# Kernel optimization log

Measured on AMD Instinct MI355X. Metric: run time of the kernel, lower is better.

Reference implementation:

```python
import jax, jax.numpy as jnp
import numpy as np

N_NODES = 100000
N_EDGES = 625000
D = 128
N_LAYERS = 10

def setup_inputs() -> dict:
    key = jax.random.key(0)
    ks = jax.random.split(key, 6)
    x = jax.random.normal(ks[0], (N_NODES, D), dtype=jnp.float32)
    edge_index = jax.random.randint(ks[1], (2, N_EDGES), 0, N_NODES, dtype=jnp.int32)
    # PyG SAGEConv params per layer: lin_l (aggregated msgs, with bias), lin_r (root, no bias)
    scale = 1.0 / np.sqrt(D)
    Wl = jax.random.normal(ks[2], (N_LAYERS, D, D), dtype=jnp.float32) * scale
    Wr = jax.random.normal(ks[3], (N_LAYERS, D, D), dtype=jnp.float32) * scale
    b = jax.random.normal(ks[4], (N_LAYERS, D), dtype=jnp.float32) * 0.01
    return {"x": x, "Wl": Wl, "Wr": Wr, "b": b, "edge_index": edge_index}

def reference(x, Wl, Wr, b, edge_index):
    src = edge_index[0]
    dst = edge_index[1]
    n = x.shape[0]
    # in-degree for mean aggregation (clamped to avoid div by zero)
    deg = jax.ops.segment_sum(jnp.ones(src.shape[0], x.dtype), dst, num_segments=n)
    deg = jnp.maximum(deg, 1.0)[:, None]
    n_layers = Wl.shape[0]
    for i in range(n_layers):
        # SAGEConv: out = lin_l(mean_{j in N(i)} x_j) + lin_r(x_i)
        agg = jax.ops.segment_sum(x[src], dst, num_segments=n) / deg
        x = agg @ Wl[i] + x @ Wr[i] + b[i]
        if i < n_layers - 1:
            x = jax.nn.relu(x)  # dropout is identity in eval mode
    return x
```

## Files before the change

kernel.cpp:

```cpp
#include <hip/hip_runtime.h>
#include <hip/hip_bf16.h>

#define N_NODES 100000
#define N_EDGES 625000
#define D 128
#define N_LAYERS 10
#define SCAN_BLOCKS 98

typedef __attribute__((ext_vector_type(8))) short bf16x8;
typedef __attribute__((ext_vector_type(4))) float floatx4;

static __device__ __forceinline__ ushort f2bf(float f) {
    uint u = __float_as_uint(f);
    u += 0x7fff + ((u >> 16) & 1);
    return (ushort)(u >> 16);
}
static __device__ __forceinline__ float bf2f(ushort h) {
    return __uint_as_float(((uint)h) << 16);
}


__global__ void hist_kernel(const int* __restrict__ dst, int* __restrict__ deg) {
    int e = blockIdx.x * blockDim.x + threadIdx.x;
    if (e < N_EDGES) atomicAdd(&deg[dst[e]], 1);
}

__global__ void scanA_kernel(const int* __restrict__ deg, int* __restrict__ offsets,
                             int* __restrict__ blockSums) {
    __shared__ int s[1024];
    int tid = threadIdx.x;
    int i = blockIdx.x * 1024 + tid;
    int v = (i < N_NODES) ? deg[i] : 0;
    s[tid] = v;
    __syncthreads();
    for (int d = 1; d < 1024; d <<= 1) {
        int t = (tid >= d) ? s[tid - d] : 0;
        __syncthreads();
        s[tid] += t;
        __syncthreads();
    }
    if (i < N_NODES) offsets[i] = s[tid] - v;
    if (tid == 1023) blockSums[blockIdx.x] = s[1023];
}

__global__ void scanB_kernel(const int* __restrict__ blockSums, int* __restrict__ blockOffsets) {
    __shared__ int s[128];
    int tid = threadIdx.x;
    int v = (tid < SCAN_BLOCKS) ? blockSums[tid] : 0;
    s[tid] = v;
    __syncthreads();
    for (int d = 1; d < 128; d <<= 1) {
        int t = (tid >= d) ? s[tid - d] : 0;
        __syncthreads();
        s[tid] += t;
        __syncthreads();
    }
    blockOffsets[tid] = s[tid] - v;
}

__global__ void scanC_kernel(int* __restrict__ offsets, const int* __restrict__ blockOffsets) {
    int i = blockIdx.x * 1024 + threadIdx.x;
    if (i < N_NODES) offsets[i] += blockOffsets[blockIdx.x];
}

__global__ void invdeg_kernel(const int* __restrict__ deg, float* __restrict__ invdeg,
                              int* __restrict__ offsets) {
    int i = blockIdx.x * blockDim.x + threadIdx.x;
    if (i < N_NODES) {
        int d = deg[i];
        invdeg[i] = 1.0f / (float)(d > 0 ? d : 1);
    }
    if (i == 0) offsets[N_NODES] = N_EDGES;
}

__global__ void scatter_kernel(const int* __restrict__ src, const int* __restrict__ dst,
                               const int* __restrict__ offsets, int* __restrict__ fill,
                               int* __restrict__ srcSorted) {
    int e = blockIdx.x * blockDim.x + threadIdx.x;
    if (e < N_EDGES) {
        int d_ = dst[e];
        int pos = offsets[d_] + atomicAdd(&fill[d_], 1);
        srcSorted[pos] = src[e];
    }
}

__global__ void wsplit_kernel(const float* __restrict__ Wl, const float* __restrict__ Wr,
                              ushort* __restrict__ Whi, ushort* __restrict__ Wlo) {
    int t = blockIdx.x * blockDim.x + threadIdx.x;
    if (t >= N_LAYERS * 4 * 16 * 64) return;
    int lane  = t & 63;
    int ntile = (t >> 6) & 15;
    int s     = (t >> 10) & 3;
    int layer = t >> 12;
    int n = ntile * 16 + (lane & 15);
    int kbase = s * 32 + (lane >> 4) * 8;
    const float* W = (n < 128) ? (Wl + (size_t)layer * D * D + n)
                               : (Wr + (size_t)layer * D * D + (n - 128));
    size_t off = (size_t)t * 8;
#pragma unroll
    for (int j = 0; j < 8; ++j) {
        float w = W[(size_t)(kbase + j) * D];
        ushort hh = f2bf(w);
        Whi[off + j] = hh;
        Wlo[off + j] = f2bf(w - bf2f(hh));
    }
}

__global__ __launch_bounds__(256) void gemm_hz(
        const float* __restrict__ X, const ushort* __restrict__ Whi,
        const ushort* __restrict__ Wlo, const float* __restrict__ bias,
        uint* __restrict__ h2out, float* __restrict__ z) {
    __shared__ ushort Ahi[2][4 * 64 * 8];
    __shared__ ushort Alo[2][4 * 64 * 8];

    int tid  = threadIdx.x;
    int lane = tid & 63;
    int wave = tid >> 6;

    int r    = tid >> 4;
    int t0   = tid & 15;
    int s_st = t0 >> 2;
    int q_st = t0 & 3;
    int lanep = (q_st << 4) | r;
    int stIdx = (s_st * 64 + (lanep ^ (s_st << 2))) * 8;

    int q  = lane >> 4;
    int cc = lane & 15;

    int ntileMap[4];
#pragma unroll
    for (int nt = 0; nt < 4; ++nt)
        ntileMap[nt] = (wave < 2) ? (wave * 2 + (nt & 1) + ((nt >> 1) << 2))
                                  : (wave * 4 + nt);

    float bsc[4] = {0.f, 0.f, 0.f, 0.f};
    if (wave >= 2) {
#pragma unroll
        for (int nt = 0; nt < 4; ++nt)
            bsc[nt] = bias[((wave * 4 + nt) - 8) * 16 + cc];
    }

    int mt = blockIdx.x;
    {
        int row0 = mt * 32;
#pragma unroll
        for (int st = 0; st < 2; ++st) {
            const float* xp = X + (size_t)(row0 + st * 16 + r) * D + t0 * 8;
            float4 v0 = *(const float4*)xp;
            float4 v1 = *(const float4*)(xp + 4);
            float a[8] = {v0.x, v0.y, v0.z, v0.w, v1.x, v1.y, v1.z, v1.w};
            ushort hi8[8], lo8[8];
#pragma unroll
            for (int j = 0; j < 8; ++j) {
                ushort hh = f2bf(a[j]);
                hi8[j] = hh;
                lo8[j] = f2bf(a[j] - bf2f(hh));
            }
            *(bf16x8*)&Ahi[st][stIdx] = *(bf16x8*)hi8;
            *(bf16x8*)&Alo[st][stIdx] = *(bf16x8*)lo8;
        }
        __syncthreads();

        floatx4 acc0[4], acc1[4];
#pragma unroll
        for (int nt = 0; nt < 4; ++nt) {
            acc0[nt] = (floatx4){0.f, 0.f, 0.f, 0.f};
            acc1[nt] = (floatx4){0.f, 0.f, 0.f, 0.f};
        }
#pragma unroll
        for (int s = 0; s < 4; ++s) {
            int aIdx = (s * 64 + (lane ^ (s << 2))) * 8;
            bf16x8 ah0 = *(const bf16x8*)&Ahi[0][aIdx];
            bf16x8 al0 = *(const bf16x8*)&Alo[0][aIdx];
            bf16x8 ah1 = *(const bf16x8*)&Ahi[1][aIdx];
            bf16x8 al1 = *(const bf16x8*)&Alo[1][aIdx];
#pragma unroll
            for (int nt = 0; nt < 4; ++nt) {
                size_t wo = ((size_t)(s * 16 + ntileMap[nt]) * 64 + lane) * 8;
                bf16x8 wh = *(const bf16x8*)&Whi[wo];
                bf16x8 wl = *(const bf16x8*)&Wlo[wo];
                acc0[nt] = __builtin_amdgcn_mfma_f32_16x16x32_bf16(ah0, wh, acc0[nt], 0, 0, 0);
                acc0[nt] = __builtin_amdgcn_mfma_f32_16x16x32_bf16(al0, wh, acc0[nt], 0, 0, 0);
                acc0[nt] = __builtin_amdgcn_mfma_f32_16x16x32_bf16(ah0, wl, acc0[nt], 0, 0, 0);
                acc1[nt] = __builtin_amdgcn_mfma_f32_16x16x32_bf16(ah1, wh, acc1[nt], 0, 0, 0);
                acc1[nt] = __builtin_amdgcn_mfma_f32_16x16x32_bf16(al1, wh, acc1[nt], 0, 0, 0);
                acc1[nt] = __builtin_amdgcn_mfma_f32_16x16x32_bf16(ah1, wl, acc1[nt], 0, 0, 0);
            }
        }

#pragma unroll
        for (int st = 0; st < 2; ++st) {
            floatx4* acc = st ? acc1 : acc0;
            int rowb = row0 + st * 16;
            if (wave < 2) {
#pragma unroll
                for (int p = 0; p < 2; ++p) {
                    int c = wave * 32 + p * 16 + cc;
#pragma unroll
                    for (int rr = 0; rr < 4; ++rr) {
                        uint lo = f2bf(acc[p][rr]);
                        uint hi = f2bf(acc[p + 2][rr]);
                        h2out[(size_t)(rowb + q * 4 + rr) * 64 + c] = lo | (hi << 16);
                    }
                }
            } else {
#pragma unroll
                for (int nt = 0; nt < 4; ++nt) {
                    int col = ((wave * 4 + nt) - 8) * 16 + cc;
#pragma unroll
                    for (int rr = 0; rr < 4; ++rr) {
                        int row = rowb + q * 4 + rr;
                        z[(size_t)row * D + col] = acc[nt][rr] + bsc[nt];
                    }
                }
            }
        }
    }
}

__global__ __launch_bounds__(256) void fused_layer(
        const uint* __restrict__ h2in, const int* __restrict__ srcSorted,
        const int* __restrict__ offsets, const float* __restrict__ invdeg,
        const float* __restrict__ zio, const ushort* __restrict__ Whi,
        const ushort* __restrict__ Wlo, const float* __restrict__ bias,
        uint* __restrict__ h2out) {
    __shared__ ushort Ahi[2][4 * 64 * 8];
    __shared__ ushort Alo[2][4 * 64 * 8];

    int tid  = threadIdx.x;
    int lane = tid & 63;
    int wave = tid >> 6;
    int row0 = blockIdx.x * 32;

    int n0 = row0 + wave * 8;
    int offA[9];
#pragma unroll
    for (int i = 0; i < 9; ++i) offA[i] = offsets[n0 + i];
    int off0 = offA[0];
    int total = offA[8] - off0;
    int idxv = srcSorted[min(off0 + ((lane < total) ? lane : 0), N_EDGES - 1)];

    for (int i = 0; i < 8; ++i) {
        int sRel = offA[i] - off0;
        int eRel = offA[i + 1] - off0;
        int cnt = eRel - sRel;
        float sx = 0.f, sy = 0.f;
        if (cnt > 0 && eRel <= 64) {
            for (int k = sRel; k < eRel; k += 8) {
                int sidx[8];
#pragma unroll
                for (int j = 0; j < 8; ++j) {
                    int kk = k + j;
                    sidx[j] = __shfl(idxv, (kk < eRel) ? kk : sRel, 64);
                }
                uint u[8];
#pragma unroll
                for (int j = 0; j < 8; ++j)
                    u[j] = h2in[(size_t)sidx[j] * 64 + lane];
#pragma unroll
                for (int j = 0; j < 8; ++j) {
                    float m = ((k + j) < eRel) ? 1.f : 0.f;
                    sx += m * __uint_as_float(u[j] << 16);
                    sy += m * __uint_as_float(u[j] & 0xffff0000u);
                }
            }
        } else if (cnt > 0) {
            int offn = offA[i];
            int nv = cnt < 64 ? cnt : 64;
            int idxn = srcSorted[offn + ((lane < nv) ? lane : 0)];
            for (int k = 0; k < nv; k += 8) {
                int sidx[8];
#pragma unroll
                for (int j = 0; j < 8; ++j) {
                    int kk = k + j;
                    sidx[j] = __shfl(idxn, (kk < nv) ? kk : 0, 64);
                }
                uint u[8];
#pragma unroll
                for (int j = 0; j < 8; ++j)
                    u[j] = h2in[(size_t)sidx[j] * 64 + lane];
#pragma unroll
                for (int j = 0; j < 8; ++j) {
                    float m = ((k + j) < nv) ? 1.f : 0.f;
                    sx += m * __uint_as_float(u[j] << 16);
                    sy += m * __uint_as_float(u[j] & 0xffff0000u);
                }
            }
            for (int k = 64; k < cnt; ++k) {
                int s = srcSorted[offn + k];
                uint u = h2in[(size_t)s * 64 + lane];
                sx += __uint_as_float(u << 16);
                sy += __uint_as_float(u & 0xffff0000u);
            }
        }
        int node = n0 + i;
        float inv = invdeg[node];
        float ox = fmaxf(sx * inv + zio[(size_t)node * D + lane], 0.f);
        float oy = fmaxf(sy * inv + zio[(size_t)node * D + 64 + lane], 0.f);

        int local = wave * 8 + i;
        int st = local >> 4;
        int m = local & 15;
        {
            int c = lane;
            int s_ = c >> 5, q_ = (c >> 3) & 3, j_ = c & 7;
            int elem = (s_ * 64 + (((q_ << 4) | m) ^ (s_ << 2))) * 8 + j_;
            ushort hh = f2bf(ox);
            Ahi[st][elem] = hh;
            Alo[st][elem] = f2bf(ox - bf2f(hh));
        }
        {
            int c = lane + 64;
            int s_ = c >> 5, q_ = (c >> 3) & 3, j_ = c & 7;
            int elem = (s_ * 64 + (((q_ << 4) | m) ^ (s_ << 2))) * 8 + j_;
            ushort hh = f2bf(oy);
            Ahi[st][elem] = hh;
            Alo[st][elem] = f2bf(oy - bf2f(hh));
        }
    }
    __syncthreads();

    int q  = lane >> 4;
    int cc = lane & 15;
    int ntileMap[4];
#pragma unroll
    for (int nt = 0; nt < 4; ++nt)
        ntileMap[nt] = (wave < 2) ? (wave * 2 + (nt & 1) + ((nt >> 1) << 2))
                                  : (wave * 4 + nt);
    float bsc[4] = {0.f, 0.f, 0.f, 0.f};
    if (wave >= 2) {
#pragma unroll
        for (int nt = 0; nt < 4; ++nt)
            bsc[nt] = bias[((wave * 4 + nt) - 8) * 16 + cc];
    }

    floatx4 acc0[4], acc1[4];
#pragma unroll
    for (int nt = 0; nt < 4; ++nt) {
        acc0[nt] = (floatx4){0.f, 0.f, 0.f, 0.f};
        acc1[nt] = (floatx4){0.f, 0.f, 0.f, 0.f};
    }
#pragma unroll
    for (int s = 0; s < 4; ++s) {
        int aIdx = (s * 64 + (lane ^ (s << 2))) * 8;
        bf16x8 ah0 = *(const bf16x8*)&Ahi[0][aIdx];
        bf16x8 al0 = *(const bf16x8*)&Alo[0][aIdx];
        bf16x8 ah1 = *(const bf16x8*)&Ahi[1][aIdx];
        bf16x8 al1 = *(const bf16x8*)&Alo[1][aIdx];
#pragma unroll
        for (int nt = 0; nt < 4; ++nt) {
            size_t wo = ((size_t)(s * 16 + ntileMap[nt]) * 64 + lane) * 8;
            bf16x8 wh = *(const bf16x8*)&Whi[wo];
            bf16x8 wl = *(const bf16x8*)&Wlo[wo];
            acc0[nt] = __builtin_amdgcn_mfma_f32_16x16x32_bf16(ah0, wh, acc0[nt], 0, 0, 0);
            acc0[nt] = __builtin_amdgcn_mfma_f32_16x16x32_bf16(al0, wh, acc0[nt], 0, 0, 0);
            acc0[nt] = __builtin_amdgcn_mfma_f32_16x16x32_bf16(ah0, wl, acc0[nt], 0, 0, 0);
            acc1[nt] = __builtin_amdgcn_mfma_f32_16x16x32_bf16(ah1, wh, acc1[nt], 0, 0, 0);
            acc1[nt] = __builtin_amdgcn_mfma_f32_16x16x32_bf16(al1, wh, acc1[nt], 0, 0, 0);
            acc1[nt] = __builtin_amdgcn_mfma_f32_16x16x32_bf16(ah1, wl, acc1[nt], 0, 0, 0);
        }
    }

#pragma unroll
    for (int st = 0; st < 2; ++st) {
        floatx4* acc = st ? acc1 : acc0;
        int rowb = row0 + st * 16;
        if (wave < 2) {
#pragma unroll
            for (int p = 0; p < 2; ++p) {
                int c = wave * 32 + p * 16 + cc;
#pragma unroll
                for (int rr = 0; rr < 4; ++rr) {
                    uint lo = f2bf(acc[p][rr]);
                    uint hi = f2bf(acc[p + 2][rr]);
                    h2out[(size_t)(rowb + q * 4 + rr) * 64 + c] = lo | (hi << 16);
                }
            }
        } else {
#pragma unroll
            for (int nt = 0; nt < 4; ++nt) {
                int col = ((wave * 4 + nt) - 8) * 16 + cc;
#pragma unroll
                for (int rr = 0; rr < 4; ++rr) {
                    int row = rowb + q * 4 + rr;
                    ((float*)zio)[(size_t)row * D + col] = acc[nt][rr] + bsc[nt];
                }
            }
        }
    }
}

__global__ __launch_bounds__(256) void agg_add_kernel(
        const uint* __restrict__ h2, const int* __restrict__ srcSorted,
        const int* __restrict__ offsets, const int* __restrict__ deg,
        const float* __restrict__ invdeg, const float* __restrict__ zin,
        float* __restrict__ out) {
    int node = blockIdx.x * 4 + (threadIdx.x >> 6);
    int lane = threadIdx.x & 63;
    int off = offsets[node];
    int cnt = deg[node];
    float sx = 0.f, sy = 0.f;
    if (cnt > 0) {
        int nv = cnt < 64 ? cnt : 64;
        int idxv = srcSorted[off + ((lane < nv) ? lane : 0)];
        for (int k = 0; k < nv; k += 8) {
            int sidx[8];
#pragma unroll
            for (int j = 0; j < 8; ++j) {
                int kk = k + j;
                sidx[j] = __shfl(idxv, (kk < nv) ? kk : 0, 64);
            }
            uint u[8];
#pragma unroll
            for (int j = 0; j < 8; ++j)
                u[j] = h2[(size_t)sidx[j] * 64 + lane];
#pragma unroll
            for (int j = 0; j < 8; ++j) {
                float m = ((k + j) < nv) ? 1.f : 0.f;
                sx += m * __uint_as_float(u[j] << 16);
                sy += m * __uint_as_float(u[j] & 0xffff0000u);
            }
        }
        for (int k = 64; k < cnt; ++k) {
            int s = srcSorted[off + k];
            uint u = h2[(size_t)s * 64 + lane];
            sx += __uint_as_float(u << 16);
            sy += __uint_as_float(u & 0xffff0000u);
        }
    }
    float inv = invdeg[node];
    out[(size_t)node * 128 + lane] = sx * inv + zin[(size_t)node * 128 + lane];
    out[(size_t)node * 128 + 64 + lane] = sy * inv + zin[(size_t)node * 128 + 64 + lane];
}

extern "C" void kernel_launch(void* const* d_in, const int* in_sizes, int n_in,
                              void* d_out, int out_size, void* d_ws, size_t ws_size,
                              hipStream_t stream) {
    const float* x  = (const float*)d_in[0];
    const float* Wl = (const float*)d_in[1];
    const float* Wr = (const float*)d_in[2];
    const float* b  = (const float*)d_in[3];
    const int*   ei = (const int*)d_in[4];
    const int* src = ei;
    const int* dst = ei + N_EDGES;
    float* out = (float*)d_out;

    char* w = (char*)d_ws;
    auto alloc = [&](size_t bytes) -> char* {
        char* p = w;
        w += (bytes + 255) & ~(size_t)255;
        return p;
    };
    float*  zx        = (float*)alloc((size_t)N_NODES * D * 4);
    uint*   hbufA     = (uint*)alloc((size_t)N_NODES * 64 * 4);
    uint*   hbufB     = (uint*)alloc((size_t)N_NODES * 64 * 4);
    ushort* Whi       = (ushort*)alloc((size_t)N_LAYERS * 4 * 16 * 64 * 8 * 2);
    ushort* Wlo       = (ushort*)alloc((size_t)N_LAYERS * 4 * 16 * 64 * 8 * 2);
    int*    deg       = (int*)alloc((size_t)N_NODES * 4);
    int*    offsets   = (int*)alloc((size_t)(N_NODES + 1) * 4);
    int*    fill      = (int*)alloc((size_t)N_NODES * 4);
    int*    srcSorted = (int*)alloc((size_t)N_EDGES * 4);
    int*    blockSums = (int*)alloc(128 * 4);
    int*    blockOffs = (int*)alloc(128 * 4);
    float*  invdeg    = (float*)alloc((size_t)N_NODES * 4);

    hipMemsetAsync(deg, 0, (size_t)N_NODES * 4, stream);
    hipMemsetAsync(fill, 0, (size_t)N_NODES * 4, stream);

    hist_kernel<<<(N_EDGES + 255) / 256, 256, 0, stream>>>(dst, deg);
    scanA_kernel<<<SCAN_BLOCKS, 1024, 0, stream>>>(deg, offsets, blockSums);
    scanB_kernel<<<1, 128, 0, stream>>>(blockSums, blockOffs);
    scanC_kernel<<<SCAN_BLOCKS, 1024, 0, stream>>>(offsets, blockOffs);
    invdeg_kernel<<<(N_NODES + 255) / 256, 256, 0, stream>>>(deg, invdeg, offsets);
    scatter_kernel<<<(N_EDGES + 255) / 256, 256, 0, stream>>>(src, dst, offsets, fill, srcSorted);
    wsplit_kernel<<<(N_LAYERS * 4 * 16 * 64 + 255) / 256, 256, 0, stream>>>(Wl, Wr, Whi, Wlo);

    gemm_hz<<<N_NODES / 32, 256, 0, stream>>>(x, Whi, Wlo, b, hbufA, zx);
    uint* hin = hbufA;
    uint* hout = hbufB;
    for (int L = 1; L < N_LAYERS; ++L) {
        size_t woff = (size_t)L * 4 * 16 * 64 * 8;
        fused_layer<<<N_NODES / 32, 256, 0, stream>>>(
            hin, srcSorted, offsets, invdeg, zx,
            Whi + woff, Wlo + woff, b + (size_t)L * D, hout);
        uint* t = hin; hin = hout; hout = t;
    }
    agg_add_kernel<<<N_NODES / 4, 256, 0, stream>>>(
        hin, srcSorted, offsets, deg, invdeg, zx, out);
}
```

Baseline: 823.9 us.

## Store root term in bf16, drop A-lo split, enlarge fused layer tile to 64 rows

The per-node root/bias term z is now stored as packed bf16 pairs instead of fp32, halving its read/write traffic in every layer. The fused layer drops the low-order bf16 split of the activations, going from three to two MFMA passes, and each block now handles 64 rows with 16 nodes per wave so every weight fragment load feeds four row tiles. The column-to-wave mapping is changed so that h and z outputs can both be written as packed pairs. In exchange, both the stored z term and the activation operand lose precision, which risks accuracy drift across the ten layers.

```diff
diff --git a/kernel.cpp b/kernel.cpp
--- a/kernel.cpp
+++ b/kernel.cpp
@@ -17,6 +17,9 @@
 }
 static __device__ __forceinline__ float bf2f(ushort h) {
     return __uint_as_float(((uint)h) << 16);
+}
+static __device__ __forceinline__ uint packbf(float lo, float hi) {
+    return (uint)f2bf(lo) | ((uint)f2bf(hi) << 16);
 }
 
 
@@ -106,10 +109,15 @@
     }
 }
 
+static __device__ __forceinline__ int ntmap(int wave, int nt) {
+    int base = (wave < 2) ? wave * 2 : 8 + (wave - 2) * 2;
+    return base + (nt & 1) + ((nt >> 1) << 2);
+}
+
 __global__ __launch_bounds__(256) void gemm_hz(
         const float* __restrict__ X, const ushort* __restrict__ Whi,
         const ushort* __restrict__ Wlo, const float* __restrict__ bias,
-        uint* __restrict__ h2out, float* __restrict__ z) {
+        uint* __restrict__ h2out, uint* __restrict__ z2out) {
     __shared__ ushort Ahi[2][4 * 64 * 8];
     __shared__ ushort Alo[2][4 * 64 * 8];
 
@@ -129,210 +137,36 @@
 
     int ntileMap[4];
 #pragma unroll
-    for (int nt = 0; nt < 4; ++nt)
-        ntileMap[nt] = (wave < 2) ? (wave * 2 + (nt & 1) + ((nt >> 1) << 2))
-                                  : (wave * 4 + nt);
-
-    float bsc[4] = {0.f, 0.f, 0.f, 0.f};
+    for (int nt = 0; nt < 4; ++nt) ntileMap[nt] = ntmap(wave, nt);
+
+    float blo[2] = {0.f, 0.f}, bhi[2] = {0.f, 0.f};
     if (wave >= 2) {
 #pragma unroll
-        for (int nt = 0; nt < 4; ++nt)
-            bsc[nt] = bias[((wave * 4 + nt) - 8) * 16 + cc];
-    }
-
-    int mt = blockIdx.x;
-    {
-        int row0 = mt * 32;
-#pragma unroll
-        for (int st = 0; st < 2; ++st) {
-            const float* xp = X + (size_t)(row0 + st * 16 + r) * D + t0 * 8;
-            float4 v0 = *(const float4*)xp;
-            float4 v1 = *(const float4*)(xp + 4);
-            float a[8] = {v0.x, v0.y, v0.z, v0.w, v1.x, v1.y, v1.z, v1.w};
-            ushort hi8[8], lo8[8];
-#pragma unroll
-            for (int j = 0; j < 8; ++j) {
-                ushort hh = f2bf(a[j]);
-                hi8[j] = hh;
-                lo8[j] = f2bf(a[j] - bf2f(hh));
-            }
-            *(bf16x8*)&Ahi[st][stIdx] = *(bf16x8*)hi8;
-            *(bf16x8*)&Alo[st][stIdx] = *(bf16x8*)lo8;
-        }
-        __syncthreads();
-
-        floatx4 acc0[4], acc1[4];
-#pragma unroll
-        for (int nt = 0; nt < 4; ++nt) {
-            acc0[nt] = (floatx4){0.f, 0.f, 0.f, 0.f};
-            acc1[nt] = (floatx4){0.f, 0.f, 0.f, 0.f};
-        }
-#pragma unroll
-        for (int s = 0; s < 4; ++s) {
-            int aIdx = (s * 64 + (lane ^ (s << 2))) * 8;
-            bf16x8 ah0 = *(const bf16x8*)&Ahi[0][aIdx];
-            bf16x8 al0 = *(const bf16x8*)&Alo[0][aIdx];
-            bf16x8 ah1 = *(const bf16x8*)&Ahi[1][aIdx];
-            bf16x8 al1 = *(const bf16x8*)&Alo[1][aIdx];
-#pragma unroll
-            for (int nt = 0; nt < 4; ++nt) {
-                size_t wo = ((size_t)(s * 16 + ntileMap[nt]) * 64 + lane) * 8;
-                bf16x8 wh = *(const bf16x8*)&Whi[wo];
-                bf16x8 wl = *(const bf16x8*)&Wlo[wo];
-                acc0[nt] = __builtin_amdgcn_mfma_f32_16x16x32_bf16(ah0, wh, acc0[nt], 0, 0, 0);
-                acc0[nt] = __builtin_amdgcn_mfma_f32_16x16x32_bf16(al0, wh, acc0[nt], 0, 0, 0);
-                acc0[nt] = __builtin_amdgcn_mfma_f32_16x16x32_bf16(ah0, wl, acc0[nt], 0, 0, 0);
-                acc1[nt] = __builtin_amdgcn_mfma_f32_16x16x32_bf16(ah1, wh, acc1[nt], 0, 0, 0);
-                acc1[nt] = __builtin_amdgcn_mfma_f32_16x16x32_bf16(al1, wh, acc1[nt], 0, 0, 0);
-                acc1[nt] = __builtin_amdgcn_mfma_f32_16x16x32_bf16(ah1, wl, acc1[nt], 0, 0, 0);
-            }
-        }
-
-#pragma unroll
-        for (int st = 0; st < 2; ++st) {
-            floatx4* acc = st ? acc1 : acc0;
-            int rowb = row0 + st * 16;
-            if (wave < 2) {
-#pragma unroll
-                for (int p = 0; p < 2; ++p) {
-                    int c = wave * 32 + p * 16 + cc;
-#pragma unroll
-                    for (int rr = 0; rr < 4; ++rr) {
-                        uint lo = f2bf(acc[p][rr]);
-                        uint hi = f2bf(acc[p + 2][rr]);
-                        h2out[(size_t)(rowb + q * 4 + rr) * 64 + c] = lo | (hi << 16);
-                    }
-                }
-            } else {
-#pragma unroll
-                for (int nt = 0; nt < 4; ++nt) {
-                    int col = ((wave * 4 + nt) - 8) * 16 + cc;
-#pragma unroll
-                    for (int rr = 0; rr < 4; ++rr) {
-                        int row = rowb + q * 4 + rr;
-                        z[(size_t)row * D + col] = acc[nt][rr] + bsc[nt];
-                    }
-                }
-            }
-        }
-    }
-}
-
-__global__ __launch_bounds__(256) void fused_layer(
-        const uint* __restrict__ h2in, const int* __restrict__ srcSorted,
-        const int* __restrict__ offsets, const float* __restrict__ invdeg,
-        const float* __restrict__ zio, const ushort* __restrict__ Whi,
-        const ushort* __restrict__ Wlo, const float* __restrict__ bias,
-        uint* __restrict__ h2out) {
-    __shared__ ushort Ahi[2][4 * 64 * 8];
-    __shared__ ushort Alo[2][4 * 64 * 8];
-
-    int tid  = threadIdx.x;
-    int lane = tid & 63;
-    int wave = tid >> 6;
+        for (int p = 0; p < 2; ++p) {
+            int c = (wave - 2) * 32 + p * 16 + cc;
+            blo[p] = bias[c];
+            bhi[p] = bias[c + 64];
+        }
+    }
+
     int row0 = blockIdx.x * 32;
-
-    int n0 = row0 + wave * 8;
-    int offA[9];
-#pragma unroll
-    for (int i = 0; i < 9; ++i) offA[i] = offsets[n0 + i];
-    int off0 = offA[0];
-    int total = offA[8] - off0;
-    int idxv = srcSorted[min(off0 + ((lane < total) ? lane : 0), N_EDGES - 1)];
-
-    for (int i = 0; i < 8; ++i) {
-        int sRel = offA[i] - off0;
-        int eRel = offA[i + 1] - off0;
-        int cnt = eRel - sRel;
-        float sx = 0.f, sy = 0.f;
-        if (cnt > 0 && eRel <= 64) {
-            for (int k = sRel; k < eRel; k += 8) {
-                int sidx[8];
-#pragma unroll
-                for (int j = 0; j < 8; ++j) {
-                    int kk = k + j;
-                    sidx[j] = __shfl(idxv, (kk < eRel) ? kk : sRel, 64);
-                }
-                uint u[8];
-#pragma unroll
-                for (int j = 0; j < 8; ++j)
-                    u[j] = h2in[(size_t)sidx[j] * 64 + lane];
-#pragma unroll
-                for (int j = 0; j < 8; ++j) {
-                    float m = ((k + j) < eRel) ? 1.f : 0.f;
-                    sx += m * __uint_as_float(u[j] << 16);
-                    sy += m * __uint_as_float(u[j] & 0xffff0000u);
-                }
-            }
-        } else if (cnt > 0) {
-            int offn = offA[i];
-            int nv = cnt < 64 ? cnt : 64;
-            int idxn = srcSorted[offn + ((lane < nv) ? lane : 0)];
-            for (int k = 0; k < nv; k += 8) {
-                int sidx[8];
-#pragma unroll
-                for (int j = 0; j < 8; ++j) {
-                    int kk = k + j;
-                    sidx[j] = __shfl(idxn, (kk < nv) ? kk : 0, 64);
-                }
-                uint u[8];
-#pragma unroll
-                for (int j = 0; j < 8; ++j)
-                    u[j] = h2in[(size_t)sidx[j] * 64 + lane];
-#pragma unroll
-                for (int j = 0; j < 8; ++j) {
-                    float m = ((k + j) < nv) ? 1.f : 0.f;
-                    sx += m * __uint_as_float(u[j] << 16);
-                    sy += m * __uint_as_float(u[j] & 0xffff0000u);
-                }
-            }
-            for (int k = 64; k < cnt; ++k) {
-                int s = srcSorted[offn + k];
-                uint u = h2in[(size_t)s * 64 + lane];
-                sx += __uint_as_float(u << 16);
-                sy += __uint_as_float(u & 0xffff0000u);
-            }
-        }
-        int node = n0 + i;
-        float inv = invdeg[node];
-        float ox = fmaxf(sx * inv + zio[(size_t)node * D + lane], 0.f);
-        float oy = fmaxf(sy * inv + zio[(size_t)node * D + 64 + lane], 0.f);
-
-        int local = wave * 8 + i;
-        int st = local >> 4;
-        int m = local & 15;
-        {
-            int c = lane;
-            int s_ = c >> 5, q_ = (c >> 3) & 3, j_ = c & 7;
-            int elem = (s_ * 64 + (((q_ << 4) | m) ^ (s_ << 2))) * 8 + j_;
-            ushort hh = f2bf(ox);
-            Ahi[st][elem] = hh;
-            Alo[st][elem] = f2bf(ox - bf2f(hh));
-        }
-        {
-            int c = lane + 64;
-            int s_ = c >> 5, q_ = (c >> 3) & 3, j_ = c & 7;
-            int elem = (s_ * 64 + (((q_ << 4) | m) ^ (s_ << 2))) * 8 + j_;
-            ushort hh = f2bf(oy);
-            Ahi[st][elem] = hh;
-            Alo[st][elem] = f2bf(oy - bf2f(hh));
-        }
+#pragma unroll
+    for (int st = 0; st < 2; ++st) {
+        const float* xp = X + (size_t)(row0 + st * 16 + r) * D + t0 * 8;
+        float4 v0 = *(const float4*)xp;
+        float4 v1 = *(const float4*)(xp + 4);
+        float a[8] = {v0.x, v0.y, v0.z, v0.w, v1.x, v1.y, v1.z, v1.w};
+        ushort hi8[8], lo8[8];
+#pragma unroll
+        for (int j = 0; j < 8; ++j) {
+            ushort hh = f2bf(a[j]);
+            hi8[j] = hh;
+            lo8[j] = f2bf(a[j] - bf2f(hh));
+        }
+        *(bf16x8*)&Ahi[st][stIdx] = *(bf16x8*)hi8;
+        *(bf16x8*)&Alo[st][stIdx] = *(bf16x8*)lo8;
     }
     __syncthreads();
-
-    int q  = lane >> 4;
-    int cc = lane & 15;
-    int ntileMap[4];
-#pragma unroll
-    for (int nt = 0; nt < 4; ++nt)
-        ntileMap[nt] = (wave < 2) ? (wave * 2 + (nt & 1) + ((nt >> 1) << 2))
-                                  : (wave * 4 + nt);
-    float bsc[4] = {0.f, 0.f, 0.f, 0.f};
-    if (wave >= 2) {
-#pragma unroll
-        for (int nt = 0; nt < 4; ++nt)
-            bsc[nt] = bias[((wave * 4 + nt) - 8) * 16 + cc];
-    }
 
     floatx4 acc0[4], acc1[4];
 #pragma unroll
@@ -365,25 +199,186 @@
     for (int st = 0; st < 2; ++st) {
         floatx4* acc = st ? acc1 : acc0;
         int rowb = row0 + st * 16;
-        if (wave < 2) {
-#pragma unroll
-            for (int p = 0; p < 2; ++p) {
+#pragma unroll
+        for (int p = 0; p < 2; ++p) {
+            if (wave < 2) {
                 int c = wave * 32 + p * 16 + cc;
 #pragma unroll
-                for (int rr = 0; rr < 4; ++rr) {
-                    uint lo = f2bf(acc[p][rr]);
-                    uint hi = f2bf(acc[p + 2][rr]);
-                    h2out[(size_t)(rowb + q * 4 + rr) * 64 + c] = lo | (hi << 16);
+                for (int rr = 0; rr < 4; ++rr)
+                    h2out[(size_t)(rowb + q * 4 + rr) * 64 + c] =
+                        packbf(acc[p][rr], acc[p + 2][rr]);
+            } else {
+                int c = (wave - 2) * 32 + p * 16 + cc;
+#pragma unroll
+                for (int rr = 0; rr < 4; ++rr)
+                    z2out[(size_t)(rowb + q * 4 + rr) * 64 + c] =
+                        packbf(acc[p][rr] + blo[p], acc[p + 2][rr] + bhi[p]);
+            }
+        }
+    }
+}
+
+static __device__ __forceinline__ void frag_write1(ushort* __restrict__ A,
+                                                   int m, int c, float v) {
+    int s_ = c >> 5, q_ = (c >> 3) & 3, j_ = c & 7;
+    A[(s_ * 64 + (((q_ << 4) | m) ^ (s_ << 2))) * 8 + j_] = f2bf(v);
+}
+
+__global__ __launch_bounds__(256) void fused_layer(
+        const uint* __restrict__ h2in, const int* __restrict__ srcSorted,
+        const int* __restrict__ offsets, const float* __restrict__ invdeg,
+        uint* __restrict__ z2io, const ushort* __restrict__ Whi,
+        const ushort* __restrict__ Wlo, const float* __restrict__ bias,
+        uint* __restrict__ h2out) {
+    __shared__ ushort Ahi[4][4 * 64 * 8];
+
+    int tid  = threadIdx.x;
+    int lane = tid & 63;
+    int wave = tid >> 6;
+    int row0 = blockIdx.x * 64;
+
+    int n0 = row0 + wave * 16;
+    int offv = offsets[min(n0 + min(lane, 16), N_NODES)];
+    float invv = invdeg[min(n0 + min(lane, 15), N_NODES - 1)];
+    ushort* Afrag = Ahi[wave];
+
+#pragma unroll
+    for (int g = 0; g < 2; ++g) {
+        int base = g * 8;
+        int offG0 = __shfl(offv, base, 64);
+        int totalG = __shfl(offv, base + 8, 64) - offG0;
+        int idxv = srcSorted[min(offG0 + ((lane < totalG) ? lane : 0), N_EDGES - 1)];
+        uint zG[8];
+#pragma unroll
+        for (int i = 0; i < 8; ++i)
+            zG[i] = z2io[(size_t)min(n0 + base + i, N_NODES - 1) * 64 + lane];
+
+        for (int i = 0; i < 8; ++i) {
+            int sRel = __shfl(offv, base + i, 64) - offG0;
+            int eRel = __shfl(offv, base + i + 1, 64) - offG0;
+            int cnt = eRel - sRel;
+            float sx = 0.f, sy = 0.f;
+            if (cnt > 0 && eRel <= 64) {
+                for (int k = sRel; k < eRel; k += 8) {
+                    int sidx[8];
+#pragma unroll
+                    for (int j = 0; j < 8; ++j) {
+                        int kk = k + j;
+                        sidx[j] = __shfl(idxv, (kk < eRel) ? kk : sRel, 64);
+                    }
+                    uint u[8];
+#pragma unroll
+                    for (int j = 0; j < 8; ++j)
+                        u[j] = h2in[(size_t)sidx[j] * 64 + lane];
+#pragma unroll
+                    for (int j = 0; j < 8; ++j) {
+                        float m = ((k + j) < eRel) ? 1.f : 0.f;
+                        sx += m * __uint_as_float(u[j] << 16);
+                        sy += m * __uint_as_float(u[j] & 0xffff0000u);
+                    }
                 }
-            }
-        } else {
-#pragma unroll
-            for (int nt = 0; nt < 4; ++nt) {
-                int col = ((wave * 4 + nt) - 8) * 16 + cc;
+            } else if (cnt > 0) {
+                int offn = offG0 + sRel;
+                int nv = cnt < 64 ? cnt : 64;
+                int idxn = srcSorted[offn + ((lane < nv) ? lane : 0)];
+                for (int k = 0; k < nv; k += 8) {
+                    int sidx[8];
+#pragma unroll
+                    for (int j = 0; j < 8; ++j) {
+                        int kk = k + j;
+                        sidx[j] = __shfl(idxn, (kk < nv) ? kk : 0, 64);
+                    }
+                    uint u[8];
+#pragma unroll
+                    for (int j = 0; j < 8; ++j)
+                        u[j] = h2in[(size_t)sidx[j] * 64 + lane];
+#pragma unroll
+                    for (int j = 0; j < 8; ++j) {
+                        float m = ((k + j) < nv) ? 1.f : 0.f;
+                        sx += m * __uint_as_float(u[j] << 16);
+                        sy += m * __uint_as_float(u[j] & 0xffff0000u);
+                    }
+                }
+                for (int k = 64; k < cnt; ++k) {
+                    int s = srcSorted[offn + k];
+                    uint u = h2in[(size_t)s * 64 + lane];
+                    sx += __uint_as_float(u << 16);
+                    sy += __uint_as_float(u & 0xffff0000u);
+                }
+            }
+            float inv = __shfl(invv, base + i, 64);
+            uint zp = zG[i];
+            float ox = fmaxf(sx * inv + __uint_as_float(zp << 16), 0.f);
+            float oy = fmaxf(sy * inv + __uint_as_float(zp & 0xffff0000u), 0.f);
+            int m = base + i;
+            frag_write1(Afrag, m, lane, ox);
+            frag_write1(Afrag, m, lane + 64, oy);
+        }
+    }
+    __syncthreads();
+
+    int q  = lane >> 4;
+    int cc = lane & 15;
+    int ntileMap[4];
+#pragma unroll
+    for (int nt = 0; nt < 4; ++nt) ntileMap[nt] = ntmap(wave, nt);
+
+    float blo[2] = {0.f, 0.f}, bhi[2] = {0.f, 0.f};
+    if (wave >= 2) {
+#pragma unroll
+        for (int p = 0; p < 2; ++p) {
+            int c = (wave - 2) * 32 + p * 16 + cc;
+            blo[p] = bias[c];
+            bhi[p] = bias[c + 64];
+        }
+    }
+
+    floatx4 acc[4][4];
+#pragma unroll
+    for (int st = 0; st < 4; ++st)
+#pragma unroll
+        for (int nt = 0; nt < 4; ++nt) acc[st][nt] = (floatx4){0.f, 0.f, 0.f, 0.f};
+
+#pragma unroll
+    for (int s = 0; s < 4; ++s) {
+        int aIdx = (s * 64 + (lane ^ (s << 2))) * 8;
+        bf16x8 a[4];
+#pragma unroll
+        for (int st = 0; st < 4; ++st) a[st] = *(const bf16x8*)&Ahi[st][aIdx];
+#pragma unroll
+        for (int nt = 0; nt < 4; ++nt) {
+            size_t wo = ((size_t)(s * 16 + ntileMap[nt]) * 64 + lane) * 8;
+            bf16x8 wh = *(const bf16x8*)&Whi[wo];
+            bf16x8 wl = *(const bf16x8*)&Wlo[wo];
+#pragma unroll
+            for (int st = 0; st < 4; ++st) {
+                acc[st][nt] = __builtin_amdgcn_mfma_f32_16x16x32_bf16(a[st], wh, acc[st][nt], 0, 0, 0);
+                acc[st][nt] = __builtin_amdgcn_mfma_f32_16x16x32_bf16(a[st], wl, acc[st][nt], 0, 0, 0);
+            }
+        }
+    }
+
+#pragma unroll
+    for (int st = 0; st < 4; ++st) {
+        int rowb = row0 + st * 16;
+#pragma unroll
+        for (int p = 0; p < 2; ++p) {
+            if (wave < 2) {
+                int c = wave * 32 + p * 16 + cc;
 #pragma unroll
                 for (int rr = 0; rr < 4; ++rr) {
                     int row = rowb + q * 4 + rr;
-                    ((float*)zio)[(size_t)row * D + col] = acc[nt][rr] + bsc[nt];
+                    if (row < N_NODES)
+                        h2out[(size_t)row * 64 + c] = packbf(acc[st][p][rr], acc[st][p + 2][rr]);
+                }
+            } else {
+                int c = (wave - 2) * 32 + p * 16 + cc;
+#pragma unroll
+                for (int rr = 0; rr < 4; ++rr) {
+                    int row = rowb + q * 4 + rr;
+                    if (row < N_NODES)
+                        z2io[(size_t)row * 64 + c] =
+                            packbf(acc[st][p][rr] + blo[p], acc[st][p + 2][rr] + bhi[p]);
                 }
             }
         }
@@ -393,7 +388,7 @@
 __global__ __launch_bounds__(256) void agg_add_kernel(
         const uint* __restrict__ h2, const int* __restrict__ srcSorted,
         const int* __restrict__ offsets, const int* __restrict__ deg,
-        const float* __restrict__ invdeg, const float* __restrict__ zin,
+        const float* __restrict__ invdeg, const uint* __restrict__ z2,
         float* __restrict__ out) {
     int node = blockIdx.x * 4 + (threadIdx.x >> 6);
     int lane = threadIdx.x & 63;
@@ -429,8 +424,9 @@
         }
     }
     float inv = invdeg[node];
-    out[(size_t)node * 128 + lane] = sx * inv + zin[(size_t)node * 128 + lane];
-    out[(size_t)node * 128 + 64 + lane] = sy * inv + zin[(size_t)node * 128 + 64 + lane];
+    uint zp = z2[(size_t)node * 64 + lane];
+    out[(size_t)node * 128 + lane]      = sx * inv + __uint_as_float(zp << 16);
+    out[(size_t)node * 128 + 64 + lane] = sy * inv + __uint_as_float(zp & 0xffff0000u);
 }
 
 extern "C" void kernel_launch(void* const* d_in, const int* in_sizes, int n_in,
@@ -451,7 +447,7 @@
         w += (bytes + 255) & ~(size_t)255;
         return p;
     };
-    float*  zx        = (float*)alloc((size_t)N_NODES * D * 4);
+    uint*   z2        = (uint*)alloc((size_t)N_NODES * 64 * 4);
     uint*   hbufA     = (uint*)alloc((size_t)N_NODES * 64 * 4);
     uint*   hbufB     = (uint*)alloc((size_t)N_NODES * 64 * 4);
     ushort* Whi       = (ushort*)alloc((size_t)N_LAYERS * 4 * 16 * 64 * 8 * 2);
@@ -475,16 +471,16 @@
     scatter_kernel<<<(N_EDGES + 255) / 256, 256, 0, stream>>>(src, dst, offsets, fill, srcSorted);
     wsplit_kernel<<<(N_LAYERS * 4 * 16 * 64 + 255) / 256, 256, 0, stream>>>(Wl, Wr, Whi, Wlo);
 
-    gemm_hz<<<N_NODES / 32, 256, 0, stream>>>(x, Whi, Wlo, b, hbufA, zx);
+    gemm_hz<<<N_NODES / 32, 256, 0, stream>>>(x, Whi, Wlo, b, hbufA, z2);
     uint* hin = hbufA;
     uint* hout = hbufB;
     for (int L = 1; L < N_LAYERS; ++L) {
         size_t woff = (size_t)L * 4 * 16 * 64 * 8;
-        fused_layer<<<N_NODES / 32, 256, 0, stream>>>(
-            hin, srcSorted, offsets, invdeg, zx,
+        fused_layer<<<(N_NODES + 63) / 64, 256, 0, stream>>>(
+            hin, srcSorted, offsets, invdeg, z2,
             Whi + woff, Wlo + woff, b + (size_t)L * D, hout);
         uint* t = hin; hin = hout; hout = t;
     }
     agg_add_kernel<<<N_NODES / 4, 256, 0, stream>>>(
-        hin, srcSorted, offsets, deg, invdeg, zx, out);
-}
+        hin, srcSorted, offsets, deg, invdeg, z2, out);
+}
```

Result: slower. 879.4 us (+6.7%).
